# Optimization experiments

Measured on AMD Instinct MI355X. Metric: run time of the kernel, lower is better.

## Reference

```python
import jax, jax.numpy as jnp
import numpy as np

H = 128          # hidden_size
EF = 2           # expansion_factor
E = H * EF       # expanded hidden size
K = 4            # conv kernel size
R = 8            # dt_rank = ceil(128/16)
L = 2            # num_layers
BATCH = 2
SEQ = 1024
EPS = 1e-5


def rmsnorm(x, w):
    return x * jax.lax.rsqrt(jnp.mean(x * x, axis=-1, keepdims=True) + EPS) * w


def causal_conv1d(x, w, b):
    # x: (b, l, E); w: (E, 1, K) depthwise; left-pad K-1 => causal, output len l
    xt = jnp.transpose(x, (0, 2, 1))  # (b, E, l)
    out = jax.lax.conv_general_dilated(
        xt, w, window_strides=(1,), padding=[(K - 1, 0)],
        dimension_numbers=("NCH", "OIH", "NCH"), feature_group_count=E)
    out = out + b[None, :, None]
    return jnp.transpose(out, (0, 2, 1))


def sscan(xc, delta, A, Bm, Cm, Dp):
    # xc, delta: (b,l,E); A: (E,n); Bm, Cm: (b,l,n); Dp: (E,)
    deltaA = jnp.exp(jnp.einsum('bld,dn->bldn', delta, A))          # (b,l,E,n)
    deltaBx = jnp.einsum('bld,bln,bld->bldn', delta, Bm, xc)        # (b,l,E,n)

    def step(h, inp):
        dA_t, dBx_t, C_t = inp           # (b,E,n), (b,E,n), (b,n)
        h = dA_t * h + dBx_t
        y = jnp.einsum('bdn,bn->bd', h, C_t)
        return h, y

    b = xc.shape[0]
    h0 = jnp.zeros((b, E, A.shape[1]), dtype=xc.dtype)
    _, ys = jax.lax.scan(
        step, h0,
        (jnp.transpose(deltaA, (1, 0, 2, 3)),
         jnp.transpose(deltaBx, (1, 0, 2, 3)),
         jnp.transpose(Cm, (1, 0, 2))))
    y = jnp.transpose(ys, (1, 0, 2))     # (b,l,E)
    return y + Dp * xc


def mamba_block(x, in_w, in_b, out_w, out_b, pl_w, pl_b, dt_w, dt_b,
                conv_w, conv_b, A_log, Dp):
    xz = x @ in_w + in_b                 # (b,l,2E)
    xc, skip = jnp.split(xz, [E], axis=-1)
    xc = jax.nn.silu(causal_conv1d(xc, conv_w, conv_b))
    # ssm
    A = -jnp.exp(A_log)                  # (E,H)
    dbc = xc @ pl_w + pl_b               # (b,l,R+2H)
    delta, Bm, Cm = jnp.split(dbc, [R, R + H], axis=-1)
    delta = jax.nn.softplus(delta @ dt_w + dt_b)   # (b,l,E)
    y = sscan(xc, delta, A, Bm, Cm, Dp)
    y = y * jax.nn.silu(skip)
    return y @ out_w + out_b


def forward(x, in_w, in_b, out_w, out_b, pl_w, pl_b, dt_w, dt_b,
            conv_w, conv_b, A_log, Dp, norm_w, final_norm_w):
    for i in range(L):
        x = mamba_block(rmsnorm(x, norm_w[i]), in_w[i], in_b[i], out_w[i],
                        out_b[i], pl_w[i], pl_b[i], dt_w[i], dt_b[i],
                        conv_w[i], conv_b[i], A_log[i], Dp[i]) + x
    return rmsnorm(x, final_norm_w)


def setup_inputs() -> dict:
    key = jax.random.key(0)
    ks = jax.random.split(key, 12)
    s = 0.02
    x = jax.random.normal(ks[0], (BATCH, SEQ, H), dtype=jnp.float32)
    in_w = jax.random.normal(ks[1], (L, H, 2 * E)) * s
    in_b = jnp.zeros((L, 2 * E))
    out_w = jax.random.normal(ks[2], (L, E, H)) * s
    out_b = jnp.zeros((L, H))
    pl_w = jax.random.normal(ks[3], (L, E, R + 2 * H)) * s
    pl_b = jnp.zeros((L, R + 2 * H))
    dt_w = jax.random.normal(ks[4], (L, R, E)) * s
    dt_b = jnp.zeros((L, E))
    conv_w = jax.random.normal(ks[5], (L, E, 1, K)) * (1.0 / np.sqrt(K))
    conv_b = jnp.zeros((L, E))
    A_log = jnp.broadcast_to(jnp.log(jnp.arange(1, H + 1, dtype=jnp.float32)),
                             (L, E, H))
    Dp = jnp.ones((L, E))
    norm_w = jnp.ones((L, H))
    final_norm_w = jnp.ones((H,))
    return {"x": x, "in_w": in_w, "in_b": in_b, "out_w": out_w,
            "out_b": out_b, "pl_w": pl_w, "pl_b": pl_b, "dt_w": dt_w,
            "dt_b": dt_b, "conv_w": conv_w, "conv_b": conv_b,
            "A_log": A_log, "Dp": Dp, "norm_w": norm_w,
            "final_norm_w": final_norm_w}


def reference(x, in_w, in_b, out_w, out_b, pl_w, pl_b, dt_w, dt_b,
              conv_w, conv_b, A_log, Dp, norm_w, final_norm_w):
    return forward(x, in_w, in_b, out_w, out_b, pl_w, pl_b, dt_w, dt_b,
                   conv_w, conv_b, A_log, Dp, norm_w, final_norm_w)
```

## Files before the change

### kernel.cpp

```cpp
#include <hip/hip_runtime.h>
#include <hip/hip_bf16.h>

#define HH 128
#define EE 256
#define KK 4
#define RR 8
#define LL 2
#define BB 2
#define SS 1024
#define BT (BB*SS)
#define NJ (RR+2*HH)
#define GG 16
#define CH (SS/GG)
#define EPS 1e-5f
#define LOG2E 1.44269504088896f

__device__ __forceinline__ float silu_f(float v) {
    return v / (1.0f + __expf(-v));
}

__global__ __launch_bounds__(512) void k_norm_inproj(
    const float* __restrict__ xin, const float* __restrict__ inw,
    const float* __restrict__ inb, const float* __restrict__ nw,
    float* __restrict__ xz)
{
    __shared__ float xn[16][128];
    const int bt0 = blockIdx.x * 16;
    const int tid = threadIdx.x;
    {
        const int t = tid >> 5, g = tid & 31;
        const float4 xv = *(const float4*)(xin + (bt0 + t) * HH + g * 4);
        float ss = xv.x*xv.x + xv.y*xv.y + xv.z*xv.z + xv.w*xv.w;
        #pragma unroll
        for (int m = 16; m >= 1; m >>= 1) ss += __shfl_xor(ss, m);
        const float rs = rsqrtf(ss * (1.0f / HH) + EPS);
        const float4 wv = *(const float4*)(nw + g * 4);
        float4 o;
        o.x = xv.x * rs * wv.x; o.y = xv.y * rs * wv.y;
        o.z = xv.z * rs * wv.z; o.w = xv.w * rs * wv.w;
        *(float4*)(&xn[t][g * 4]) = o;
    }
    __syncthreads();
    const int j = tid;
    float acc[16];
    const float bj = inb[j];
    #pragma unroll
    for (int t = 0; t < 16; t++) acc[t] = bj;
    float w0n = inw[0*512 + j], w1n = inw[1*512 + j];
    float w2n = inw[2*512 + j], w3n = inw[3*512 + j];
    for (int k4 = 0; k4 < 32; k4++) {
        const float w0 = w0n, w1 = w1n, w2 = w2n, w3 = w3n;
        if (k4 < 31) {
            const int k = (k4 + 1) * 4;
            w0n = inw[(k+0)*512 + j]; w1n = inw[(k+1)*512 + j];
            w2n = inw[(k+2)*512 + j]; w3n = inw[(k+3)*512 + j];
        }
        const int k = k4 * 4;
        #pragma unroll
        for (int t = 0; t < 16; t++) {
            const float4 xv = *(const float4*)(&xn[t][k]);
            acc[t] += w0*xv.x + w1*xv.y + w2*xv.z + w3*xv.w;
        }
    }
    #pragma unroll
    for (int t = 0; t < 16; t++) xz[(bt0 + t) * 512 + j] = acc[t];
}

__global__ __launch_bounds__(512) void k_fused_cpd(
    const float* __restrict__ xz, const float* __restrict__ cw,
    const float* __restrict__ cb, const float* __restrict__ plw,
    const float* __restrict__ plb, const float* __restrict__ dtw,
    const float* __restrict__ dtb,
    float* __restrict__ xcT, float* __restrict__ BC4,
    float* __restrict__ deltaT, float* __restrict__ sT)
{
    __shared__ float xcb[16][256];
    __shared__ float dbc[8][16];
    const int bt0 = blockIdx.x * 16;
    const int tid = threadIdx.x;
    {
        const int e = tid & 255, hf = tid >> 8;
        const int ts = bt0 + hf * 8;
        const float w0 = cw[e*4+0], w1 = cw[e*4+1], w2 = cw[e*4+2], w3 = cw[e*4+3];
        const float bias = cb[e];
        const float* xp = xz + (size_t)ts * 512 + e;
        const bool first = ((ts & 1023) == 0);
        float xm3 = first ? 0.0f : xp[-3*512];
        float xm2 = first ? 0.0f : xp[-2*512];
        float xm1 = first ? 0.0f : xp[-1*512];
        float xcv[8];
        #pragma unroll
        for (int i = 0; i < 8; i++) {
            const float x0 = xp[i*512];
            const float v = bias + w3*x0 + w2*xm1 + w1*xm2 + w0*xm3;
            const float o = silu_f(v);
            xcv[i] = o;
            xcb[hf*8 + i][e] = o;
            xm3 = xm2; xm2 = xm1; xm1 = x0;
        }
        float* orow = xcT + (size_t)e * BT + ts;
        *(float4*)(orow)     = make_float4(xcv[0], xcv[1], xcv[2], xcv[3]);
        *(float4*)(orow + 4) = make_float4(xcv[4], xcv[5], xcv[6], xcv[7]);
    }
    __syncthreads();
    if (tid < NJ) {
        const int j = tid;
        float acc[16];
        const float bj = plb[j];
        #pragma unroll
        for (int t = 0; t < 16; t++) acc[t] = bj;
        float w0n = plw[0*NJ + j], w1n = plw[1*NJ + j];
        float w2n = plw[2*NJ + j], w3n = plw[3*NJ + j];
        for (int e4 = 0; e4 < 64; e4++) {
            const float w0 = w0n, w1 = w1n, w2 = w2n, w3 = w3n;
            if (e4 < 63) {
                const int e = (e4 + 1) * 4;
                w0n = plw[(e+0)*NJ + j]; w1n = plw[(e+1)*NJ + j];
                w2n = plw[(e+2)*NJ + j]; w3n = plw[(e+3)*NJ + j];
            }
            const int e = e4 * 4;
            #pragma unroll
            for (int t = 0; t < 16; t++) {
                const float4 xv = *(const float4*)(&xcb[t][e]);
                acc[t] += w0*xv.x + w1*xv.y + w2*xv.z + w3*xv.w;
            }
        }
        if (j < RR) {
            #pragma unroll
            for (int t = 0; t < 16; t++) dbc[j][t] = acc[t];
        } else {
            const int isC = (j >= RR + HH);
            const int nn = isC ? (j - RR - HH) : (j - RR);
            const int tq0 = bt0 >> 2;
            #pragma unroll
            for (int q = 0; q < 4; q++) {
                float* p = BC4 + ((size_t)(tq0 + q) * 128 + nn) * 8 + (isC ? 4 : 0);
                *(float4*)p = make_float4(acc[q*4+0], acc[q*4+1], acc[q*4+2], acc[q*4+3]);
            }
        }
    }
    __syncthreads();
    {
        const int e = tid & 255, hf = tid >> 8;
        const int ts = bt0 + hf * 8;
        float dv[8];
        const float db = dtb[e];
        #pragma unroll
        for (int i = 0; i < 8; i++) dv[i] = db;
        #pragma unroll
        for (int r = 0; r < RR; r++) {
            const float w = dtw[r*EE + e];
            #pragma unroll
            for (int i = 0; i < 8; i++) dv[i] += w * dbc[r][hf*8 + i];
        }
        float spv[8], sv[8];
        #pragma unroll
        for (int i = 0; i < 8; i++) {
            const float d = dv[i];
            const float sp = (d > 15.0f) ? d : log1pf(__expf(d));
            spv[i] = sp;
            sv[i] = sp * xcb[hf*8 + i][e];
        }
        float* drp = deltaT + (size_t)e * BT + ts;
        *(float4*)(drp)     = make_float4(spv[0], spv[1], spv[2], spv[3]);
        *(float4*)(drp + 4) = make_float4(spv[4], spv[5], spv[6], spv[7]);
        float* srp = sT + (size_t)e * BT + ts;
        *(float4*)(srp)     = make_float4(sv[0], sv[1], sv[2], sv[3]);
        *(float4*)(srp + 4) = make_float4(sv[4], sv[5], sv[6], sv[7]);
    }
}

__global__ __launch_bounds__(128, 4) void k_scan_local(
    const float* __restrict__ BC4, const float* __restrict__ deltaT,
    const float* __restrict__ sT, const float* __restrict__ Alog,
    float* __restrict__ yT, float* __restrict__ hchain,
    float* __restrict__ dsum)
{
    __shared__ float part[2][16][68];
    __shared__ float ybuf[2][CH];
    const int blk = blockIdx.x;
    const int wgid = (blk & 7) * 512 + (blk >> 3);
    const int eq = wgid & 127;
    const int r0 = wgid >> 7;
    const int b = r0 >> 4;
    const int g = r0 & 15;
    const int e0 = eq * 2;
    const int n = threadIdx.x;
    const int t0 = g * CH;

    float An0 = -__expf(Alog[(e0+0) * HH + n]) * LOG2E;
    float An1 = -__expf(Alog[(e0+1) * HH + n]) * LOG2E;
    float h0 = 0.0f, h1 = 0.0f, cum0 = 0.0f, cum1 = 0.0f;
    const float* bc = BC4 + ((size_t)((b * 256 + g * 16) * 128 + n)) * 8;
    const float* dr0 = deltaT + (size_t)(e0+0) * BT + b * SS + t0;
    const float* dr1 = deltaT + (size_t)(e0+1) * BT + b * SS + t0;
    const float* sr0 = sT + (size_t)(e0+0) * BT + b * SS + t0;
    const float* sr1 = sT + (size_t)(e0+1) * BT + b * SS + t0;

    float4 pB = *(const float4*)(bc);
    float4 pC = *(const float4*)(bc + 4);
    float4 pd0 = *(const float4*)dr0, pd1 = *(const float4*)dr1;
    float4 ps0 = *(const float4*)sr0, ps1 = *(const float4*)sr1;

    const int tl = n >> 3, jj = n & 7;
    for (int sc = 0; sc < 4; sc++) {
        #pragma unroll
        for (int q = 0; q < 4; q++) {
            const int qq = sc * 4 + q;
            const float4 cB = pB, cC = pC;
            const float4 cd0 = pd0, cd1 = pd1, cs0 = ps0, cs1 = ps1;
            if (qq < 15) {
                const size_t off = (size_t)(qq + 1) * 1024;
                pB = *(const float4*)(bc + off);
                pC = *(const float4*)(bc + off + 4);
                const int t = (qq + 1) * 4;
                pd0 = *(const float4*)(dr0 + t); pd1 = *(const float4*)(dr1 + t);
                ps0 = *(const float4*)(sr0 + t); ps1 = *(const float4*)(sr1 + t);
            }
            float a;
            a = exp2f(cd0.x*An0); h0 = a*h0 + cs0.x*cB.x; part[0][q*4+0][n] = h0*cC.x;
            a = exp2f(cd0.y*An0); h0 = a*h0 + cs0.y*cB.y; part[0][q*4+1][n] = h0*cC.y;
            a = exp2f(cd0.z*An0); h0 = a*h0 + cs0.z*cB.z; part[0][q*4+2][n] = h0*cC.z;
            a = exp2f(cd0.w*An0); h0 = a*h0 + cs0.w*cB.w; part[0][q*4+3][n] = h0*cC.w;
            a = exp2f(cd1.x*An1); h1 = a*h1 + cs1.x*cB.x; part[1][q*4+0][n] = h1*cC.x;
            a = exp2f(cd1.y*An1); h1 = a*h1 + cs1.y*cB.y; part[1][q*4+1][n] = h1*cC.y;
            a = exp2f(cd1.z*An1); h1 = a*h1 + cs1.z*cB.z; part[1][q*4+2][n] = h1*cC.z;
            a = exp2f(cd1.w*An1); h1 = a*h1 + cs1.w*cB.w; part[1][q*4+3][n] = h1*cC.w;
            cum0 += (cd0.x + cd0.y) + (cd0.z + cd0.w);
            cum1 += (cd1.x + cd1.y) + (cd1.z + cd1.w);
        }
        __syncthreads();
        #pragma unroll
        for (int ee = 0; ee < 2; ee++) {
            float s0 = 0, s1 = 0, s2 = 0, s3 = 0;
            #pragma unroll
            for (int i = 0; i < 4; i++) {
                const float4 p = *(const float4*)(&part[ee][tl][jj*16 + i*4]);
                s0 += p.x; s1 += p.y; s2 += p.z; s3 += p.w;
            }
            float r = (s0 + s1) + (s2 + s3);
            r += __shfl_xor(r, 1); r += __shfl_xor(r, 2); r += __shfl_xor(r, 4);
            if (jj == 0) ybuf[ee][sc*16 + tl] = r;
        }
        __syncthreads();
    }
    {
        const int ee = n >> 6, tt = n & 63;
        yT[(size_t)(e0 + ee) * BT + b * SS + t0 + tt] = ybuf[ee][tt];
    }
    hchain[(size_t)(((b * EE + e0 + 0) * GG) + g) * 128 + n] = h0;
    hchain[(size_t)(((b * EE + e0 + 1) * GG) + g) * 128 + n] = h1;
    if (n == 0) {
        dsum[(b * EE + e0 + 0) * GG + g] = cum0;
        dsum[(b * EE + e0 + 1) * GG + g] = cum1;
    }
}

__global__ __launch_bounds__(128, 4) void k_scan_fix(
    const float* __restrict__ BC4, const float* __restrict__ deltaT,
    const float* __restrict__ Alog, const float* __restrict__ hchain,
    const float* __restrict__ dsum, float* __restrict__ yT)
{
    __shared__ float part[2][16][68];
    __shared__ float ybuf[2][CH];
    const int blk = blockIdx.x;
    const int wgid = (blk & 7) * 480 + (blk >> 3);
    const int eq = wgid & 127;
    const int r0 = wgid >> 7;
    const int b = r0 / 15;
    const int g = 1 + (r0 % 15);
    const int e0 = eq * 2;
    const int n = threadIdx.x;
    const int t0 = g * CH;

    const float An0 = -__expf(Alog[(e0+0) * HH + n]) * LOG2E;
    const float An1 = -__expf(Alog[(e0+1) * HH + n]) * LOG2E;
    float w0 = 0.0f, w1 = 0.0f;
    {
        const size_t hb0 = (size_t)((b * EE + e0 + 0) * GG) * 128 + n;
        const size_t hb1 = (size_t)((b * EE + e0 + 1) * GG) * 128 + n;
        const int db0 = (b * EE + e0 + 0) * GG;
        const int db1 = (b * EE + e0 + 1) * GG;
        for (int gp = 0; gp < g; gp++) {
            const float he0 = hchain[hb0 + (size_t)gp * 128];
            const float he1 = hchain[hb1 + (size_t)gp * 128];
            w0 = exp2f(An0 * dsum[db0 + gp]) * w0 + he0;
            w1 = exp2f(An1 * dsum[db1 + gp]) * w1 + he1;
        }
    }
    float D0 = 0.0f, D1 = 0.0f;
    const float* bc = BC4 + ((size_t)((b * 256 + g * 16) * 128 + n)) * 8;
    const float* dr0 = deltaT + (size_t)(e0+0) * BT + b * SS + t0;
    const float* dr1 = deltaT + (size_t)(e0+1) * BT + b * SS + t0;

    float4 pC = *(const float4*)(bc + 4);
    float4 pd0 = *(const float4*)dr0, pd1 = *(const float4*)dr1;

    const int tl = n >> 3, jj = n & 7;
    for (int sc = 0; sc < 4; sc++) {
        #pragma unroll
        for (int q = 0; q < 4; q++) {
            const int qq = sc * 4 + q;
            const float4 cC = pC;
            const float4 cd0 = pd0, cd1 = pd1;
            if (qq < 15) {
                const size_t off = (size_t)(qq + 1) * 1024;
                pC = *(const float4*)(bc + off + 4);
                const int t = (qq + 1) * 4;
                pd0 = *(const float4*)(dr0 + t); pd1 = *(const float4*)(dr1 + t);
            }
            D0 += cd0.x; part[0][q*4+0][n] = exp2f(An0*D0) * w0 * cC.x;
            D0 += cd0.y; part[0][q*4+1][n] = exp2f(An0*D0) * w0 * cC.y;
            D0 += cd0.z; part[0][q*4+2][n] = exp2f(An0*D0) * w0 * cC.z;
            D0 += cd0.w; part[0][q*4+3][n] = exp2f(An0*D0) * w0 * cC.w;
            D1 += cd1.x; part[1][q*4+0][n] = exp2f(An1*D1) * w1 * cC.x;
            D1 += cd1.y; part[1][q*4+1][n] = exp2f(An1*D1) * w1 * cC.y;
            D1 += cd1.z; part[1][q*4+2][n] = exp2f(An1*D1) * w1 * cC.z;
            D1 += cd1.w; part[1][q*4+3][n] = exp2f(An1*D1) * w1 * cC.w;
        }
        __syncthreads();
        #pragma unroll
        for (int ee = 0; ee < 2; ee++) {
            float s0 = 0, s1 = 0, s2 = 0, s3 = 0;
            #pragma unroll
            for (int i = 0; i < 4; i++) {
                const float4 p = *(const float4*)(&part[ee][tl][jj*16 + i*4]);
                s0 += p.x; s1 += p.y; s2 += p.z; s3 += p.w;
            }
            float r = (s0 + s1) + (s2 + s3);
            r += __shfl_xor(r, 1); r += __shfl_xor(r, 2); r += __shfl_xor(r, 4);
            if (jj == 0) ybuf[ee][sc*16 + tl] = r;
        }
        __syncthreads();
    }
    {
        const int ee = n >> 6, tt = n & 63;
        yT[(size_t)(e0 + ee) * BT + b * SS + t0 + tt] += ybuf[ee][tt];
    }
}

template<int NEXT, int FINAL>
__global__ __launch_bounds__(256) void k_gate(
    const float* __restrict__ yT, const float* __restrict__ xcT,
    const float* __restrict__ xz, const float* __restrict__ Dp,
    const float* __restrict__ ow, const float* __restrict__ ob,
    const float* __restrict__ resin, float* __restrict__ xres,
    const float* __restrict__ nw, const float* __restrict__ inw,
    const float* __restrict__ inb, float* __restrict__ xznext,
    const float* __restrict__ fw, float* __restrict__ out)
{
    __shared__ float gs[16][256];
    __shared__ float rb[16][132];
    const int bt0 = blockIdx.x * 16;
    const int tid = threadIdx.x;
    {
        const int e = tid;
        const float dp = Dp[e];
        const float* yp = yT + (size_t)e * BT + bt0;
        const float* xp = xcT + (size_t)e * BT + bt0;
        #pragma unroll
        for (int tq = 0; tq < 4; tq++) {
            const float4 y4 = *(const float4*)(yp + tq * 4);
            const float4 x4 = *(const float4*)(xp + tq * 4);
            float sk;
            sk = xz[(size_t)(bt0 + tq*4 + 0) * 512 + 256 + e];
            gs[tq*4+0][e] = (y4.x + dp * x4.x) * silu_f(sk);
            sk = xz[(size_t)(bt0 + tq*4 + 1) * 512 + 256 + e];
            gs[tq*4+1][e] = (y4.y + dp * x4.y) * silu_f(sk);
            sk = xz[(size_t)(bt0 + tq*4 + 2) * 512 + 256 + e];
            gs[tq*4+2][e] = (y4.z + dp * x4.z) * silu_f(sk);
            sk = xz[(size_t)(bt0 + tq*4 + 3) * 512 + 256 + e];
            gs[tq*4+3][e] = (y4.w + dp * x4.w) * silu_f(sk);
        }
    }
    __syncthreads();
    const int j = tid & 127;
    const int kh = tid >> 7;
    {
        float acc[16];
        #pragma unroll
        for (int t = 0; t < 16; t++) acc[t] = 0.0f;
        const int eb = kh * 128;
        float w0n = ow[(eb+0)*HH + j], w1n = ow[(eb+1)*HH + j];
        float w2n = ow[(eb+2)*HH + j], w3n = ow[(eb+3)*HH + j];
        for (int e4 = 0; e4 < 32; e4++) {
            const float w0 = w0n, w1 = w1n, w2 = w2n, w3 = w3n;
            if (e4 < 31) {
                const int e = eb + (e4 + 1) * 4;
                w0n = ow[(e+0)*HH + j]; w1n = ow[(e+1)*HH + j];
                w2n = ow[(e+2)*HH + j]; w3n = ow[(e+3)*HH + j];
            }
            const int e = eb + e4 * 4;
            #pragma unroll
            for (int t = 0; t < 16; t++) {
                const float4 g4 = *(const float4*)(&gs[t][e]);
                acc[t] += w0*g4.x + w1*g4.y + w2*g4.z + w3*g4.w;
            }
        }
        if (kh == 1) {
            #pragma unroll
            for (int t = 0; t < 16; t++) rb[t][j] = acc[t];
        }
        __syncthreads();
        if (kh == 0) {
            const float bj = ob[j];
            #pragma unroll
            for (int t = 0; t < 16; t++) {
                const float r = acc[t] + rb[t][j] + bj
                              + resin[(size_t)(bt0 + t) * HH + j];
                if (!FINAL) xres[(size_t)(bt0 + t) * HH + j] = r;
                rb[t][j] = r;
            }
        }
    }
    if (NEXT || FINAL) {
        __syncthreads();
        const int t = tid >> 4, g16 = tid & 15;
        const float4 a = *(const float4*)(&rb[t][g16*8]);
        const float4 c = *(const float4*)(&rb[t][g16*8 + 4]);
        float ss = a.x*a.x + a.y*a.y + a.z*a.z + a.w*a.w
                 + c.x*c.x + c.y*c.y + c.z*c.z + c.w*c.w;
        ss += __shfl_xor(ss, 1); ss += __shfl_xor(ss, 2);
        ss += __shfl_xor(ss, 4); ss += __shfl_xor(ss, 8);
        if (g16 == 0) rb[t][128] = rsqrtf(ss * (1.0f / HH) + EPS);
        __syncthreads();
    }
    if (FINAL) {
        const int jc = tid & 127, th = tid >> 7;
        const float fwj = fw[jc];
        #pragma unroll
        for (int i = 0; i < 8; i++) {
            const int t = th * 8 + i;
            out[(size_t)(bt0 + t) * HH + jc] = rb[t][jc] * rb[t][128] * fwj;
        }
    }
    if (NEXT) {
        const int j0 = tid, j1 = tid + 256;
        float acc0[16], acc1[16];
        #pragma unroll
        for (int t = 0; t < 16; t++) { acc0[t] = 0.0f; acc1[t] = 0.0f; }
        for (int k4 = 0; k4 < 32; k4++) {
            const int k = k4 * 4;
            const float4 nv = *(const float4*)(nw + k);
            const float u0 = inw[(k+0)*512 + j0] * nv.x;
            const float u1 = inw[(k+1)*512 + j0] * nv.y;
            const float u2 = inw[(k+2)*512 + j0] * nv.z;
            const float u3 = inw[(k+3)*512 + j0] * nv.w;
            const float v0 = inw[(k+0)*512 + j1] * nv.x;
            const float v1 = inw[(k+1)*512 + j1] * nv.y;
            const float v2 = inw[(k+2)*512 + j1] * nv.z;
            const float v3 = inw[(k+3)*512 + j1] * nv.w;
            #pragma unroll
            for (int t = 0; t < 16; t++) {
                const float4 xv = *(const float4*)(&rb[t][k]);
                acc0[t] += u0*xv.x + u1*xv.y + u2*xv.z + u3*xv.w;
                acc1[t] += v0*xv.x + v1*xv.y + v2*xv.z + v3*xv.w;
            }
        }
        const float b0 = inb[j0], b1 = inb[j1];
        #pragma unroll
        for (int t = 0; t < 16; t++) {
            const float rs = rb[t][128];
            xznext[(size_t)(bt0 + t) * 512 + j0] = acc0[t] * rs + b0;
            xznext[(size_t)(bt0 + t) * 512 + j1] = acc1[t] * rs + b1;
        }
    }
}

extern "C" void kernel_launch(void* const* d_in, const int* in_sizes, int n_in,
                              void* d_out, int out_size, void* d_ws, size_t ws_size,
                              hipStream_t stream)
{
    const float* x      = (const float*)d_in[0];
    const float* in_w   = (const float*)d_in[1];
    const float* in_b   = (const float*)d_in[2];
    const float* out_w  = (const float*)d_in[3];
    const float* out_b  = (const float*)d_in[4];
    const float* pl_w   = (const float*)d_in[5];
    const float* pl_b   = (const float*)d_in[6];
    const float* dt_w   = (const float*)d_in[7];
    const float* dt_b   = (const float*)d_in[8];
    const float* conv_w = (const float*)d_in[9];
    const float* conv_b = (const float*)d_in[10];
    const float* A_log  = (const float*)d_in[11];
    const float* Dp     = (const float*)d_in[12];
    const float* norm_w = (const float*)d_in[13];
    const float* fnw    = (const float*)d_in[14];

    float* ws     = (float*)d_ws;
    float* xres   = ws;
    float* xz     = xres   + 262144;
    float* xcT    = xz     + 1048576;
    float* BC4    = xcT    + 524288;
    float* deltaT = BC4    + 524288;
    float* sT     = deltaT + 524288;
    float* yT     = sT     + 524288;
    float* hchain = yT     + 524288;
    float* dsum   = hchain + 1048576;

    k_norm_inproj<<<BT/16, 512, 0, stream>>>(x, in_w, in_b, norm_w, xz);
    k_fused_cpd<<<BT/16, 512, 0, stream>>>(
        xz, conv_w, conv_b, pl_w, pl_b, dt_w, dt_b, xcT, BC4, deltaT, sT);
    k_scan_local<<<BB*GG*(EE/2), 128, 0, stream>>>(
        BC4, deltaT, sT, A_log, yT, hchain, dsum);
    k_scan_fix<<<BB*(GG-1)*(EE/2), 128, 0, stream>>>(
        BC4, deltaT, A_log, hchain, dsum, yT);
    k_gate<1, 0><<<BT/16, 256, 0, stream>>>(
        yT, xcT, xz, Dp, out_w, out_b, x, xres,
        norm_w + HH, in_w + (size_t)HH*2*EE, in_b + 2*EE, xz,
        nullptr, nullptr);

    k_fused_cpd<<<BT/16, 512, 0, stream>>>(
        xz, conv_w + EE*KK, conv_b + EE, pl_w + (size_t)EE*NJ, pl_b + NJ,
        dt_w + RR*EE, dt_b + EE, xcT, BC4, deltaT, sT);
    k_scan_local<<<BB*GG*(EE/2), 128, 0, stream>>>(
        BC4, deltaT, sT, A_log + (size_t)EE*HH, yT, hchain, dsum);
    k_scan_fix<<<BB*(GG-1)*(EE/2), 128, 0, stream>>>(
        BC4, deltaT, A_log + (size_t)EE*HH, hchain, dsum, yT);
    k_gate<0, 1><<<BT/16, 256, 0, stream>>>(
        yT, xcT, xz, Dp + EE, out_w + (size_t)EE*HH, out_b + HH, xres, xres,
        nullptr, nullptr, nullptr, nullptr,
        fnw, (float*)d_out);
}
```

Measured before the change: 267.1 us.

## Fold dt projection into combined weight, unfuse gate/inproj, halve row tiles

Precomputes a fused E×E weight (pl_w[:, :R] @ dt_w) and bias in a small kernel, so delta is produced by one 256-wide GEMV path running in parallel with the B/C projection. This removes the serial low-rank step and its extra barrier. The fused next-layer in-projection and final norm are split back out of the gate kernel into separate kernels, adding launches and an xres round-trip. Row tiles drop from 16 to 8 per block, doubling block counts but also doubling weight re-reads per row. The folded delta weight does about 16x more multiply-adds per row than the rank-8 path.

New measurement: 231.3 us. 13.4% less time.

```diff
diff --git a/kernel.cpp b/kernel.cpp
--- a/kernel.cpp
+++ b/kernel.cpp
@@ -19,33 +19,58 @@
     return v / (1.0f + __expf(-v));
 }
 
+__global__ __launch_bounds__(256) void k_wdt(
+    const float* __restrict__ plw, const float* __restrict__ plb,
+    const float* __restrict__ dtw, const float* __restrict__ dtb,
+    float* __restrict__ Wdt, float* __restrict__ bdt)
+{
+    const int l = blockIdx.x >> 2, q = blockIdx.x & 3;
+    const int j = threadIdx.x;
+    const float* dtwl = dtw + (size_t)l * RR * EE;
+    const float* plwl = plw + (size_t)l * EE * NJ;
+    float wr[RR];
+    #pragma unroll
+    for (int r = 0; r < RR; r++) wr[r] = dtwl[r * EE + j];
+    float* Wl = Wdt + (size_t)l * EE * EE;
+    for (int e = q * 64; e < q * 64 + 64; e++) {
+        float a = 0.0f;
+        #pragma unroll
+        for (int r = 0; r < RR; r++) a += plwl[(size_t)e * NJ + r] * wr[r];
+        Wl[(size_t)e * EE + j] = a;
+    }
+    if (q == 0) {
+        float a = dtb[l * EE + j];
+        #pragma unroll
+        for (int r = 0; r < RR; r++) a += plb[l * NJ + r] * wr[r];
+        bdt[l * EE + j] = a;
+    }
+}
+
 __global__ __launch_bounds__(512) void k_norm_inproj(
     const float* __restrict__ xin, const float* __restrict__ inw,
     const float* __restrict__ inb, const float* __restrict__ nw,
     float* __restrict__ xz)
 {
-    __shared__ float xn[16][128];
-    const int bt0 = blockIdx.x * 16;
+    __shared__ float xn[8][128];
+    const int bt0 = blockIdx.x * 8;
     const int tid = threadIdx.x;
     {
-        const int t = tid >> 5, g = tid & 31;
-        const float4 xv = *(const float4*)(xin + (bt0 + t) * HH + g * 4);
-        float ss = xv.x*xv.x + xv.y*xv.y + xv.z*xv.z + xv.w*xv.w;
-        #pragma unroll
-        for (int m = 16; m >= 1; m >>= 1) ss += __shfl_xor(ss, m);
+        const int t = tid >> 6, lane = tid & 63;
+        const float2 xv = *(const float2*)(xin + (size_t)(bt0 + t) * HH + lane * 2);
+        float ss = xv.x*xv.x + xv.y*xv.y;
+        #pragma unroll
+        for (int m = 32; m >= 1; m >>= 1) ss += __shfl_xor(ss, m);
         const float rs = rsqrtf(ss * (1.0f / HH) + EPS);
-        const float4 wv = *(const float4*)(nw + g * 4);
-        float4 o;
-        o.x = xv.x * rs * wv.x; o.y = xv.y * rs * wv.y;
-        o.z = xv.z * rs * wv.z; o.w = xv.w * rs * wv.w;
-        *(float4*)(&xn[t][g * 4]) = o;
+        const float2 wv = *(const float2*)(nw + lane * 2);
+        xn[t][lane*2+0] = xv.x * rs * wv.x;
+        xn[t][lane*2+1] = xv.y * rs * wv.y;
     }
     __syncthreads();
     const int j = tid;
-    float acc[16];
+    float acc[8];
     const float bj = inb[j];
     #pragma unroll
-    for (int t = 0; t < 16; t++) acc[t] = bj;
+    for (int t = 0; t < 8; t++) acc[t] = bj;
     float w0n = inw[0*512 + j], w1n = inw[1*512 + j];
     float w2n = inw[2*512 + j], w3n = inw[3*512 + j];
     for (int k4 = 0; k4 < 32; k4++) {
@@ -57,114 +82,111 @@
         }
         const int k = k4 * 4;
         #pragma unroll
-        for (int t = 0; t < 16; t++) {
+        for (int t = 0; t < 8; t++) {
             const float4 xv = *(const float4*)(&xn[t][k]);
             acc[t] += w0*xv.x + w1*xv.y + w2*xv.z + w3*xv.w;
         }
     }
     #pragma unroll
-    for (int t = 0; t < 16; t++) xz[(bt0 + t) * 512 + j] = acc[t];
-}
-
-__global__ __launch_bounds__(512) void k_fused_cpd(
+    for (int t = 0; t < 8; t++) xz[(size_t)(bt0 + t) * 512 + j] = acc[t];
+}
+
+__global__ __launch_bounds__(512) void k_cbd(
     const float* __restrict__ xz, const float* __restrict__ cw,
     const float* __restrict__ cb, const float* __restrict__ plw,
-    const float* __restrict__ plb, const float* __restrict__ dtw,
-    const float* __restrict__ dtb,
+    const float* __restrict__ plb, const float* __restrict__ Wdt,
+    const float* __restrict__ bdt,
     float* __restrict__ xcT, float* __restrict__ BC4,
     float* __restrict__ deltaT, float* __restrict__ sT)
 {
-    __shared__ float xcb[16][256];
-    __shared__ float dbc[8][16];
-    const int bt0 = blockIdx.x * 16;
+    __shared__ float xcb[8][256];
+    const int bt0 = blockIdx.x * 8;
     const int tid = threadIdx.x;
     {
         const int e = tid & 255, hf = tid >> 8;
-        const int ts = bt0 + hf * 8;
+        const int ts = bt0 + hf * 4;
         const float w0 = cw[e*4+0], w1 = cw[e*4+1], w2 = cw[e*4+2], w3 = cw[e*4+3];
         const float bias = cb[e];
         const float* xp = xz + (size_t)ts * 512 + e;
-        const bool first = ((ts & 1023) == 0);
+        const bool first = ((ts & (SS-1)) == 0);
         float xm3 = first ? 0.0f : xp[-3*512];
         float xm2 = first ? 0.0f : xp[-2*512];
         float xm1 = first ? 0.0f : xp[-1*512];
-        float xcv[8];
-        #pragma unroll
-        for (int i = 0; i < 8; i++) {
+        float xcv[4];
+        #pragma unroll
+        for (int i = 0; i < 4; i++) {
             const float x0 = xp[i*512];
             const float v = bias + w3*x0 + w2*xm1 + w1*xm2 + w0*xm3;
             const float o = silu_f(v);
             xcv[i] = o;
-            xcb[hf*8 + i][e] = o;
+            xcb[hf*4 + i][e] = o;
             xm3 = xm2; xm2 = xm1; xm1 = x0;
         }
-        float* orow = xcT + (size_t)e * BT + ts;
-        *(float4*)(orow)     = make_float4(xcv[0], xcv[1], xcv[2], xcv[3]);
-        *(float4*)(orow + 4) = make_float4(xcv[4], xcv[5], xcv[6], xcv[7]);
+        *(float4*)(xcT + (size_t)e * BT + ts) =
+            make_float4(xcv[0], xcv[1], xcv[2], xcv[3]);
     }
     __syncthreads();
-    if (tid < NJ) {
-        const int j = tid;
-        float acc[16];
-        const float bj = plb[j];
-        #pragma unroll
-        for (int t = 0; t < 16; t++) acc[t] = bj;
-        float w0n = plw[0*NJ + j], w1n = plw[1*NJ + j];
-        float w2n = plw[2*NJ + j], w3n = plw[3*NJ + j];
+    const int j = tid & 255, path = tid >> 8;
+    if (path == 0) {
+        const int nn = j & 127, isC = j >> 7;
+        const float* wp = plw + RR + isC * HH + nn;
+        float acc[8];
+        const float bj = plb[RR + isC * HH + nn];
+        #pragma unroll
+        for (int t = 0; t < 8; t++) acc[t] = bj;
+        float w0n = wp[0*NJ], w1n = wp[1*NJ], w2n = wp[2*NJ], w3n = wp[3*NJ];
         for (int e4 = 0; e4 < 64; e4++) {
             const float w0 = w0n, w1 = w1n, w2 = w2n, w3 = w3n;
             if (e4 < 63) {
                 const int e = (e4 + 1) * 4;
-                w0n = plw[(e+0)*NJ + j]; w1n = plw[(e+1)*NJ + j];
-                w2n = plw[(e+2)*NJ + j]; w3n = plw[(e+3)*NJ + j];
+                w0n = wp[(size_t)(e+0)*NJ]; w1n = wp[(size_t)(e+1)*NJ];
+                w2n = wp[(size_t)(e+2)*NJ]; w3n = wp[(size_t)(e+3)*NJ];
             }
             const int e = e4 * 4;
             #pragma unroll
-            for (int t = 0; t < 16; t++) {
+            for (int t = 0; t < 8; t++) {
                 const float4 xv = *(const float4*)(&xcb[t][e]);
                 acc[t] += w0*xv.x + w1*xv.y + w2*xv.z + w3*xv.w;
             }
         }
-        if (j < RR) {
+        const int tq0 = bt0 >> 2;
+        float* p0 = BC4 + ((size_t)tq0 * 128 + nn) * 8 + isC * 4;
+        *(float4*)p0 = make_float4(acc[0], acc[1], acc[2], acc[3]);
+        float* p1 = BC4 + ((size_t)(tq0 + 1) * 128 + nn) * 8 + isC * 4;
+        *(float4*)p1 = make_float4(acc[4], acc[5], acc[6], acc[7]);
+    } else {
+        const float* wp = Wdt + j;
+        float acc[8];
+        const float bj = bdt[j];
+        #pragma unroll
+        for (int t = 0; t < 8; t++) acc[t] = bj;
+        float w0n = wp[0*EE], w1n = wp[1*EE], w2n = wp[2*EE], w3n = wp[3*EE];
+        for (int e4 = 0; e4 < 64; e4++) {
+            const float w0 = w0n, w1 = w1n, w2 = w2n, w3 = w3n;
+            if (e4 < 63) {
+                const int e = (e4 + 1) * 4;
+                w0n = wp[(size_t)(e+0)*EE]; w1n = wp[(size_t)(e+1)*EE];
+                w2n = wp[(size_t)(e+2)*EE]; w3n = wp[(size_t)(e+3)*EE];
+            }
+            const int e = e4 * 4;
             #pragma unroll
-            for (int t = 0; t < 16; t++) dbc[j][t] = acc[t];
-        } else {
-            const int isC = (j >= RR + HH);
-            const int nn = isC ? (j - RR - HH) : (j - RR);
-            const int tq0 = bt0 >> 2;
-            #pragma unroll
-            for (int q = 0; q < 4; q++) {
-                float* p = BC4 + ((size_t)(tq0 + q) * 128 + nn) * 8 + (isC ? 4 : 0);
-                *(float4*)p = make_float4(acc[q*4+0], acc[q*4+1], acc[q*4+2], acc[q*4+3]);
-            }
-        }
-    }
-    __syncthreads();
-    {
-        const int e = tid & 255, hf = tid >> 8;
-        const int ts = bt0 + hf * 8;
-        float dv[8];
-        const float db = dtb[e];
-        #pragma unroll
-        for (int i = 0; i < 8; i++) dv[i] = db;
-        #pragma unroll
-        for (int r = 0; r < RR; r++) {
-            const float w = dtw[r*EE + e];
-            #pragma unroll
-            for (int i = 0; i < 8; i++) dv[i] += w * dbc[r][hf*8 + i];
+            for (int t = 0; t < 8; t++) {
+                const float4 xv = *(const float4*)(&xcb[t][e]);
+                acc[t] += w0*xv.x + w1*xv.y + w2*xv.z + w3*xv.w;
+            }
         }
         float spv[8], sv[8];
         #pragma unroll
-        for (int i = 0; i < 8; i++) {
-            const float d = dv[i];
+        for (int t = 0; t < 8; t++) {
+            const float d = acc[t];
             const float sp = (d > 15.0f) ? d : log1pf(__expf(d));
-            spv[i] = sp;
-            sv[i] = sp * xcb[hf*8 + i][e];
-        }
-        float* drp = deltaT + (size_t)e * BT + ts;
+            spv[t] = sp;
+            sv[t] = sp * xcb[t][j];
+        }
+        float* drp = deltaT + (size_t)j * BT + bt0;
         *(float4*)(drp)     = make_float4(spv[0], spv[1], spv[2], spv[3]);
         *(float4*)(drp + 4) = make_float4(spv[4], spv[5], spv[6], spv[7]);
-        float* srp = sT + (size_t)e * BT + ts;
+        float* srp = sT + (size_t)j * BT + bt0;
         *(float4*)(srp)     = make_float4(sv[0], sv[1], sv[2], sv[3]);
         *(float4*)(srp + 4) = make_float4(sv[4], sv[5], sv[6], sv[7]);
     }
@@ -339,19 +361,15 @@
     }
 }
 
-template<int NEXT, int FINAL>
 __global__ __launch_bounds__(256) void k_gate(
     const float* __restrict__ yT, const float* __restrict__ xcT,
     const float* __restrict__ xz, const float* __restrict__ Dp,
     const float* __restrict__ ow, const float* __restrict__ ob,
-    const float* __restrict__ resin, float* __restrict__ xres,
-    const float* __restrict__ nw, const float* __restrict__ inw,
-    const float* __restrict__ inb, float* __restrict__ xznext,
-    const float* __restrict__ fw, float* __restrict__ out)
-{
-    __shared__ float gs[16][256];
-    __shared__ float rb[16][132];
-    const int bt0 = blockIdx.x * 16;
+    const float* __restrict__ resin, float* __restrict__ xres)
+{
+    __shared__ float gs[8][256];
+    __shared__ float p2[8][128];
+    const int bt0 = blockIdx.x * 8;
     const int tid = threadIdx.x;
     {
         const int e = tid;
@@ -359,7 +377,7 @@
         const float* yp = yT + (size_t)e * BT + bt0;
         const float* xp = xcT + (size_t)e * BT + bt0;
         #pragma unroll
-        for (int tq = 0; tq < 4; tq++) {
+        for (int tq = 0; tq < 2; tq++) {
             const float4 y4 = *(const float4*)(yp + tq * 4);
             const float4 x4 = *(const float4*)(xp + tq * 4);
             float sk;
@@ -376,95 +394,57 @@
     __syncthreads();
     const int j = tid & 127;
     const int kh = tid >> 7;
-    {
-        float acc[16];
-        #pragma unroll
-        for (int t = 0; t < 16; t++) acc[t] = 0.0f;
-        const int eb = kh * 128;
-        float w0n = ow[(eb+0)*HH + j], w1n = ow[(eb+1)*HH + j];
-        float w2n = ow[(eb+2)*HH + j], w3n = ow[(eb+3)*HH + j];
-        for (int e4 = 0; e4 < 32; e4++) {
-            const float w0 = w0n, w1 = w1n, w2 = w2n, w3 = w3n;
-            if (e4 < 31) {
-                const int e = eb + (e4 + 1) * 4;
-                w0n = ow[(e+0)*HH + j]; w1n = ow[(e+1)*HH + j];
-                w2n = ow[(e+2)*HH + j]; w3n = ow[(e+3)*HH + j];
-            }
-            const int e = eb + e4 * 4;
-            #pragma unroll
-            for (int t = 0; t < 16; t++) {
-                const float4 g4 = *(const float4*)(&gs[t][e]);
-                acc[t] += w0*g4.x + w1*g4.y + w2*g4.z + w3*g4.w;
-            }
-        }
-        if (kh == 1) {
-            #pragma unroll
-            for (int t = 0; t < 16; t++) rb[t][j] = acc[t];
-        }
-        __syncthreads();
-        if (kh == 0) {
-            const float bj = ob[j];
-            #pragma unroll
-            for (int t = 0; t < 16; t++) {
-                const float r = acc[t] + rb[t][j] + bj
-                              + resin[(size_t)(bt0 + t) * HH + j];
-                if (!FINAL) xres[(size_t)(bt0 + t) * HH + j] = r;
-                rb[t][j] = r;
-            }
-        }
-    }
-    if (NEXT || FINAL) {
-        __syncthreads();
-        const int t = tid >> 4, g16 = tid & 15;
-        const float4 a = *(const float4*)(&rb[t][g16*8]);
-        const float4 c = *(const float4*)(&rb[t][g16*8 + 4]);
-        float ss = a.x*a.x + a.y*a.y + a.z*a.z + a.w*a.w
-                 + c.x*c.x + c.y*c.y + c.z*c.z + c.w*c.w;
-        ss += __shfl_xor(ss, 1); ss += __shfl_xor(ss, 2);
-        ss += __shfl_xor(ss, 4); ss += __shfl_xor(ss, 8);
-        if (g16 == 0) rb[t][128] = rsqrtf(ss * (1.0f / HH) + EPS);
-        __syncthreads();
-    }
-    if (FINAL) {
-        const int jc = tid & 127, th = tid >> 7;
-        const float fwj = fw[jc];
-        #pragma unroll
-        for (int i = 0; i < 8; i++) {
-            const int t = th * 8 + i;
-            out[(size_t)(bt0 + t) * HH + jc] = rb[t][jc] * rb[t][128] * fwj;
-        }
-    }
-    if (NEXT) {
-        const int j0 = tid, j1 = tid + 256;
-        float acc0[16], acc1[16];
-        #pragma unroll
-        for (int t = 0; t < 16; t++) { acc0[t] = 0.0f; acc1[t] = 0.0f; }
-        for (int k4 = 0; k4 < 32; k4++) {
-            const int k = k4 * 4;
-            const float4 nv = *(const float4*)(nw + k);
-            const float u0 = inw[(k+0)*512 + j0] * nv.x;
-            const float u1 = inw[(k+1)*512 + j0] * nv.y;
-            const float u2 = inw[(k+2)*512 + j0] * nv.z;
-            const float u3 = inw[(k+3)*512 + j0] * nv.w;
-            const float v0 = inw[(k+0)*512 + j1] * nv.x;
-            const float v1 = inw[(k+1)*512 + j1] * nv.y;
-            const float v2 = inw[(k+2)*512 + j1] * nv.z;
-            const float v3 = inw[(k+3)*512 + j1] * nv.w;
-            #pragma unroll
-            for (int t = 0; t < 16; t++) {
-                const float4 xv = *(const float4*)(&rb[t][k]);
-                acc0[t] += u0*xv.x + u1*xv.y + u2*xv.z + u3*xv.w;
-                acc1[t] += v0*xv.x + v1*xv.y + v2*xv.z + v3*xv.w;
-            }
-        }
-        const float b0 = inb[j0], b1 = inb[j1];
-        #pragma unroll
-        for (int t = 0; t < 16; t++) {
-            const float rs = rb[t][128];
-            xznext[(size_t)(bt0 + t) * 512 + j0] = acc0[t] * rs + b0;
-            xznext[(size_t)(bt0 + t) * 512 + j1] = acc1[t] * rs + b1;
-        }
-    }
+    float acc[8];
+    #pragma unroll
+    for (int t = 0; t < 8; t++) acc[t] = 0.0f;
+    const int eb = kh * 128;
+    float w0n = ow[(eb+0)*HH + j], w1n = ow[(eb+1)*HH + j];
+    float w2n = ow[(eb+2)*HH + j], w3n = ow[(eb+3)*HH + j];
+    for (int e4 = 0; e4 < 32; e4++) {
+        const float w0 = w0n, w1 = w1n, w2 = w2n, w3 = w3n;
+        if (e4 < 31) {
+            const int e = eb + (e4 + 1) * 4;
+            w0n = ow[(e+0)*HH + j]; w1n = ow[(e+1)*HH + j];
+            w2n = ow[(e+2)*HH + j]; w3n = ow[(e+3)*HH + j];
+        }
+        const int e = eb + e4 * 4;
+        #pragma unroll
+        for (int t = 0; t < 8; t++) {
+            const float4 g4 = *(const float4*)(&gs[t][e]);
+            acc[t] += w0*g4.x + w1*g4.y + w2*g4.z + w3*g4.w;
+        }
+    }
+    if (kh == 1) {
+        #pragma unroll
+        for (int t = 0; t < 8; t++) p2[t][j] = acc[t];
+    }
+    __syncthreads();
+    if (kh == 0) {
+        const float bj = ob[j];
+        #pragma unroll
+        for (int t = 0; t < 8; t++) {
+            const float r = acc[t] + p2[t][j] + bj
+                          + resin[(size_t)(bt0 + t) * HH + j];
+            xres[(size_t)(bt0 + t) * HH + j] = r;
+        }
+    }
+}
+
+__global__ __launch_bounds__(512) void k_finalnorm(
+    const float* __restrict__ xres, const float* __restrict__ fw,
+    float* __restrict__ out)
+{
+    const int bt0 = blockIdx.x * 8;
+    const int tid = threadIdx.x;
+    const int t = tid >> 6, lane = tid & 63;
+    const float2 v = *(const float2*)(xres + (size_t)(bt0 + t) * HH + lane * 2);
+    float ss = v.x*v.x + v.y*v.y;
+    #pragma unroll
+    for (int m = 32; m >= 1; m >>= 1) ss += __shfl_xor(ss, m);
+    const float rs = rsqrtf(ss * (1.0f / HH) + EPS);
+    const float2 w = *(const float2*)(fw + lane * 2);
+    float2 o; o.x = v.x * rs * w.x; o.y = v.y * rs * w.y;
+    *(float2*)(out + (size_t)(bt0 + t) * HH + lane * 2) = o;
 }
 
 extern "C" void kernel_launch(void* const* d_in, const int* in_sizes, int n_in,
@@ -497,28 +477,28 @@
     float* yT     = sT     + 524288;
     float* hchain = yT     + 524288;
     float* dsum   = hchain + 1048576;
-
-    k_norm_inproj<<<BT/16, 512, 0, stream>>>(x, in_w, in_b, norm_w, xz);
-    k_fused_cpd<<<BT/16, 512, 0, stream>>>(
-        xz, conv_w, conv_b, pl_w, pl_b, dt_w, dt_b, xcT, BC4, deltaT, sT);
-    k_scan_local<<<BB*GG*(EE/2), 128, 0, stream>>>(
-        BC4, deltaT, sT, A_log, yT, hchain, dsum);
-    k_scan_fix<<<BB*(GG-1)*(EE/2), 128, 0, stream>>>(
-        BC4, deltaT, A_log, hchain, dsum, yT);
-    k_gate<1, 0><<<BT/16, 256, 0, stream>>>(
-        yT, xcT, xz, Dp, out_w, out_b, x, xres,
-        norm_w + HH, in_w + (size_t)HH*2*EE, in_b + 2*EE, xz,
-        nullptr, nullptr);
-
-    k_fused_cpd<<<BT/16, 512, 0, stream>>>(
-        xz, conv_w + EE*KK, conv_b + EE, pl_w + (size_t)EE*NJ, pl_b + NJ,
-        dt_w + RR*EE, dt_b + EE, xcT, BC4, deltaT, sT);
-    k_scan_local<<<BB*GG*(EE/2), 128, 0, stream>>>(
-        BC4, deltaT, sT, A_log + (size_t)EE*HH, yT, hchain, dsum);
-    k_scan_fix<<<BB*(GG-1)*(EE/2), 128, 0, stream>>>(
-        BC4, deltaT, A_log + (size_t)EE*HH, hchain, dsum, yT);
-    k_gate<0, 1><<<BT/16, 256, 0, stream>>>(
-        yT, xcT, xz, Dp + EE, out_w + (size_t)EE*HH, out_b + HH, xres, xres,
-        nullptr, nullptr, nullptr, nullptr,
-        fnw, (float*)d_out);
-}
+    float* Wdt    = dsum   + 8192;
+    float* bdt    = Wdt    + 131072;
+
+    k_wdt<<<2*4, 256, 0, stream>>>(pl_w, pl_b, dt_w, dt_b, Wdt, bdt);
+
+    for (int l = 0; l < LL; l++) {
+        const float* resin = (l == 0) ? x : xres;
+        k_norm_inproj<<<BT/8, 512, 0, stream>>>(
+            resin, in_w + (size_t)l*HH*2*EE, in_b + (size_t)l*2*EE,
+            norm_w + (size_t)l*HH, xz);
+        k_cbd<<<BT/8, 512, 0, stream>>>(
+            xz, conv_w + (size_t)l*EE*KK, conv_b + (size_t)l*EE,
+            pl_w + (size_t)l*EE*NJ, pl_b + (size_t)l*NJ,
+            Wdt + (size_t)l*EE*EE, bdt + (size_t)l*EE,
+            xcT, BC4, deltaT, sT);
+        k_scan_local<<<BB*GG*(EE/2), 128, 0, stream>>>(
+            BC4, deltaT, sT, A_log + (size_t)l*EE*HH, yT, hchain, dsum);
+        k_scan_fix<<<BB*(GG-1)*(EE/2), 128, 0, stream>>>(
+            BC4, deltaT, A_log + (size_t)l*EE*HH, hchain, dsum, yT);
+        k_gate<<<BT/8, 256, 0, stream>>>(
+            yT, xcT, xz, Dp + (size_t)l*EE,
+            out_w + (size_t)l*EE*HH, out_b + (size_t)l*HH, resin, xres);
+    }
+    k_finalnorm<<<BT/8, 512, 0, stream>>>(xres, fnw, (float*)d_out);
+}
```
